# Kernel tuning notes

Measured on AMD Instinct MI355X. Metric: run time of the kernel, lower is better.

Reference implementation:

```python
import jax, jax.numpy as jnp
import numpy as np

N = 100000      # num POIs (nodes)
M = 20000       # num trajectories (hyperedges)
NNZ = 1000000   # incidence entries
D = 128         # emb_dim
NUM_LAYERS = 3
NEG_SLOPE = 0.2  # PyG HypergraphConv leaky_relu default


def setup_inputs() -> dict:
    key = jax.random.key(0)
    ks = jax.random.split(key, 8)
    pois_embs = jax.random.normal(ks[0], (N, D), jnp.float32)
    traj_embs = jax.random.normal(ks[1], (M, D), jnp.float32)
    hyperedge_weight = jax.random.uniform(ks[2], (M,), jnp.float32)
    node_idx = jax.random.randint(ks[3], (NNZ,), 0, N, jnp.int32)
    edge_idx = jax.random.randint(ks[4], (NNZ,), 0, M, jnp.int32)
    # learned params of the shared HypergraphConv layer (heads=1, concat)
    W_lin = jax.random.normal(ks[5], (D, D), jnp.float32) / np.sqrt(D).astype(np.float32)
    att = jax.random.normal(ks[6], (2 * D,), jnp.float32) * 0.1
    bias = jnp.zeros((D,), jnp.float32)
    return dict(pois_embs=pois_embs, traj_embs=traj_embs,
                hyperedge_weight=hyperedge_weight,
                node_idx=node_idx, edge_idx=edge_idx,
                W_lin=W_lin, att=att, bias=bias)


def _segment_softmax(scores, seg, num_seg):
    smax = jax.ops.segment_max(scores, seg, num_segments=num_seg)
    smax = jnp.where(jnp.isfinite(smax), smax, 0.0)  # guard empty segments
    ex = jnp.exp(scores - smax[seg])
    den = jax.ops.segment_sum(ex, seg, num_segments=num_seg)
    return ex / (den[seg] + 1e-16)


def _hconv(x, traj_embs, hyperedge_weight, node_idx, edge_idx, W_lin, att, bias):
    # x: [N, D] node feats; traj_embs: [M, D] hyperedge feats
    xt = x @ W_lin            # [N, D]  lin(x)
    et = traj_embs @ W_lin    # [M, D]  lin(hyperedge_attr)
    # attention logits per incidence pair (additive decomposition of cat*att)
    s_n = xt @ att[:D]        # [N]
    s_e = et @ att[D:]        # [M]
    alpha = jax.nn.leaky_relu(s_n[node_idx] + s_e[edge_idx], NEG_SLOPE)  # [NNZ]
    alpha = _segment_softmax(alpha, node_idx, N)  # softmax grouped by node
    # degree normalizations: D = sum_e H_ve * w_e, B = |e|
    Ddeg = jax.ops.segment_sum(hyperedge_weight[edge_idx], node_idx, num_segments=N)
    Dinv = jnp.where(Ddeg > 0, 1.0 / Ddeg, 0.0)
    Bdeg = jax.ops.segment_sum(jnp.ones((NNZ,), xt.dtype), edge_idx, num_segments=M)
    Binv = jnp.where(Bdeg > 0, 1.0 / Bdeg, 0.0)
    # node -> edge: B^{-1} H^T (alpha * x)
    msg1 = (alpha * Binv[edge_idx])[:, None] * xt[node_idx]        # [NNZ, D]
    edge_out = jax.ops.segment_sum(msg1, edge_idx, num_segments=M)  # [M, D]
    # edge -> node: D^{-1} H (alpha * edge_out)
    msg2 = (alpha * Dinv[node_idx])[:, None] * edge_out[edge_idx]   # [NNZ, D]
    out = jax.ops.segment_sum(msg2, node_idx, num_segments=N)       # [N, D]
    return out + bias


def reference(pois_embs, traj_embs, hyperedge_weight, node_idx, edge_idx, W_lin, att, bias):
    cur = pois_embs
    acc = pois_embs  # running sum of stacked layer outputs (incl. input)
    for _ in range(NUM_LAYERS):
        cur = _hconv(cur, traj_embs, hyperedge_weight, node_idx, edge_idx, W_lin, att, bias) + cur
        acc = acc + cur
    return acc / jnp.asarray(NUM_LAYERS + 1, acc.dtype)  # mean over stack
```

## Files before the change

kernel.cpp:

```cpp
#include <hip/hip_runtime.h>
#include <cstdint>
#include <cstddef>

#define DIM 128
#define NEG_SLOPE 0.2f

#define EREP 16
#define NREP 8

typedef __attribute__((ext_vector_type(8))) short short8v;
typedef __attribute__((ext_vector_type(4))) float float4v;

__device__ __forceinline__ float bf_lo(uint u) { return __uint_as_float(u << 16); }
__device__ __forceinline__ float bf_hi(uint u) { return __uint_as_float(u & 0xffff0000u); }
__device__ __forceinline__ uint f2bf(float f) {
  uint u = __float_as_uint(f);
  return (u + 0x7fffu + ((u >> 16) & 1u)) >> 16;
}
__device__ __forceinline__ uint pack_bf2(float lo, float hi) {
  return f2bf(lo) | (f2bf(hi) << 16);
}
__device__ __forceinline__ float lrelu(float x) {
  return x >= 0.0f ? x : NEG_SLOPE * x;
}

__global__ void wswz_kernel(const float* __restrict__ W, ushort* __restrict__ Wswz)
{
  int i = blockIdx.x * 256 + threadIdx.x;
  int j = i & 7, lane = (i >> 3) & 63, nt = (i >> 9) & 7, kt = i >> 12;
  int k = kt * 32 + (lane >> 4) * 8 + j;
  int col = nt * 16 + (lane & 15);
  Wswz[i] = (ushort)f2bf(W[k * 128 + col]);
}

__global__ void poisbf_kernel(const float* __restrict__ pois,
                              uint4* __restrict__ pois_bf, int N_, int NP)
{
  int i = blockIdx.x * 256 + threadIdx.x;
  if (i >= NP * 16) return;
  int row = i >> 4;
  uint4 o;
  if (row < N_) {
    const float* src = pois + (size_t)i * 8;
    float4 f0 = *(const float4*)src;
    float4 f1 = *(const float4*)(src + 4);
    o.x = pack_bf2(f0.x, f0.y); o.y = pack_bf2(f0.z, f0.w);
    o.z = pack_bf2(f1.x, f1.y); o.w = pack_bf2(f1.z, f1.w);
  } else { o.x = o.y = o.z = o.w = 0; }
  pois_bf[i] = o;
}

__global__ __launch_bounds__(256) void gemm_mfma_kernel(
    const ushort* __restrict__ Xb, const ushort* __restrict__ Wswz,
    const float* __restrict__ att, ushort* __restrict__ Yb,
    float* __restrict__ s_n, int rowsN)
{
  __shared__ ushort st[64 * 128];
  int tid = threadIdx.x;
  int w = tid >> 6, lane = tid & 63;
  int q = lane >> 4, c = lane & 15;
  int r0b = blockIdx.x * 64;
  int r0 = r0b + w * 16;
  float4v acc[8];
#pragma unroll
  for (int nt = 0; nt < 8; ++nt) acc[nt] = (float4v){0.f, 0.f, 0.f, 0.f};
  const ushort* arow = Xb + (size_t)(r0 + c) * DIM + q * 8;
#pragma unroll
  for (int kt = 0; kt < 4; ++kt) {
    short8v a = *(const short8v*)(arow + kt * 32);
#pragma unroll
    for (int nt = 0; nt < 8; ++nt) {
      short8v b = *(const short8v*)(Wswz + ((((kt << 3) + nt) << 9) + (lane << 3)));
      acc[nt] = __builtin_amdgcn_mfma_f32_16x16x32_bf16(a, b, acc[nt], 0, 0, 0);
    }
  }
  float av[8];
#pragma unroll
  for (int nt = 0; nt < 8; ++nt) av[nt] = att[nt * 16 + c];
  float p0 = 0, p1 = 0, p2 = 0, p3 = 0;
#pragma unroll
  for (int nt = 0; nt < 8; ++nt) {
    p0 = fmaf(acc[nt][0], av[nt], p0);
    p1 = fmaf(acc[nt][1], av[nt], p1);
    p2 = fmaf(acc[nt][2], av[nt], p2);
    p3 = fmaf(acc[nt][3], av[nt], p3);
  }
#pragma unroll
  for (int m = 8; m >= 1; m >>= 1) {
    p0 += __shfl_xor(p0, m, 64);
    p1 += __shfl_xor(p1, m, 64);
    p2 += __shfl_xor(p2, m, 64);
    p3 += __shfl_xor(p3, m, 64);
  }
  if (c == 0) {
    int rb = r0 + q * 4;
    if (rb + 0 < rowsN) s_n[rb + 0] = p0;
    if (rb + 1 < rowsN) s_n[rb + 1] = p1;
    if (rb + 2 < rowsN) s_n[rb + 2] = p2;
    if (rb + 3 < rowsN) s_n[rb + 3] = p3;
  }
  ushort* sw = st + w * 2048;
#pragma unroll
  for (int nt = 0; nt < 8; ++nt) {
    sw[(q * 4 + 0) * 128 + nt * 16 + c] = (ushort)f2bf(acc[nt][0]);
    sw[(q * 4 + 1) * 128 + nt * 16 + c] = (ushort)f2bf(acc[nt][1]);
    sw[(q * 4 + 2) * 128 + nt * 16 + c] = (ushort)f2bf(acc[nt][2]);
    sw[(q * 4 + 3) * 128 + nt * 16 + c] = (ushort)f2bf(acc[nt][3]);
  }
  __syncthreads();
#pragma unroll
  for (int it = 0; it < 4; ++it) {
    int idx = tid + it * 256;
    int row = idx >> 4, seg = idx & 15;
    *(uint4*)(Yb + (size_t)(r0b + row) * DIM + seg * 8) =
        *(const uint4*)&st[row * 128 + seg * 8];
  }
}

__global__ __launch_bounds__(256) void se_kernel(
    const float* __restrict__ traj, const float* __restrict__ W,
    const float* __restrict__ att, const float* __restrict__ hw,
    float* __restrict__ s_e, float2* __restrict__ se_hw, int M_)
{
  __shared__ float wv[128];
  int tid = threadIdx.x;
  if (tid < 128) {
    const float* wr = W + (size_t)tid * 128;
    float acc = 0.0f;
#pragma unroll 4
    for (int k = 0; k < 128; ++k) acc = fmaf(wr[k], att[DIM + k], acc);
    wv[tid] = acc;
  }
  __syncthreads();
  int e = blockIdx.x * 4 + (tid >> 6);
  int lane = tid & 63;
  if (e >= M_) return;
  const float* row = traj + (size_t)e * DIM;
  float v = row[lane] * wv[lane] + row[lane + 64] * wv[lane + 64];
#pragma unroll
  for (int d = 32; d > 0; d >>= 1) v += __shfl_down(v, d, 64);
  if (lane == 0) {
    s_e[e] = v;
    float2 g; g.x = v; g.y = hw[e];
    se_hw[e] = g;
  }
}

__global__ void hist_rank_kernel(const int* __restrict__ node_idx,
                                 const int* __restrict__ edge_idx,
                                 int* __restrict__ ncnt_r, int* __restrict__ ecnt_r,
                                 int* __restrict__ r_n, int* __restrict__ r_e,
                                 int nnz, int M_, int N_)
{
  int t = blockIdx.x * blockDim.x + threadIdx.x;
  int j = t * 2;
  if (j >= nnz) return;
  int* ec = ecnt_r + (size_t)(t & (EREP - 1)) * M_;
  int* nc = ncnt_r + (size_t)(t & (NREP - 1)) * N_;
  if (j + 2 <= nnz) {
    int2 e = *(const int2*)&edge_idx[j];
    int2 n = *(const int2*)&node_idx[j];
    int a0 = atomicAdd(&ec[e.x], 1);
    int a1 = atomicAdd(&ec[e.y], 1);
    int b0 = atomicAdd(&nc[n.x], 1);
    int b1 = atomicAdd(&nc[n.y], 1);
    *(int2*)&r_e[j] = make_int2(a0, a1);
    *(int2*)&r_n[j] = make_int2(b0, b1);
  } else {
    r_e[j] = atomicAdd(&ec[edge_idx[j]], 1);
    r_n[j] = atomicAdd(&nc[node_idx[j]], 1);
  }
}

__global__ void repsum_kernel(int* __restrict__ cnt_r, int* __restrict__ cnt,
                              int nbins, int reps)
{
  int b = blockIdx.x * blockDim.x + threadIdx.x;
  if (b >= nbins) return;
  int s = 0;
  for (int r = 0; r < reps; ++r) {
    size_t o = (size_t)r * nbins + b;
    int v = cnt_r[o];
    cnt_r[o] = s;
    s += v;
  }
  cnt[b] = s;
}

__global__ __launch_bounds__(1024) void scan_block_kernel(
    const int* __restrict__ cnt, int* __restrict__ off,
    int* __restrict__ partials, int nbins)
{
  __shared__ int ws[16];
  int tid = threadIdx.x, lane = tid & 63, wid = tid >> 6;
  int base = blockIdx.x * 4096 + tid * 4;
  int x0 = base + 0 < nbins ? cnt[base + 0] : 0;
  int x1 = base + 1 < nbins ? cnt[base + 1] : 0;
  int x2 = base + 2 < nbins ? cnt[base + 2] : 0;
  int x3 = base + 3 < nbins ? cnt[base + 3] : 0;
  int t = x0 + x1 + x2 + x3;
  int v = t;
#pragma unroll
  for (int d = 1; d < 64; d <<= 1) {
    int y = __shfl_up(v, d, 64);
    if (lane >= d) v += y;
  }
  if (lane == 63) ws[wid] = v;
  __syncthreads();
  if (tid < 16) {
    int s = ws[tid];
#pragma unroll
    for (int d = 1; d < 16; d <<= 1) {
      int y = __shfl_up(s, d, 16);
      if (tid >= d) s += y;
    }
    ws[tid] = s;
  }
  __syncthreads();
  int pre = (wid > 0 ? ws[wid - 1] : 0) + (v - t);
  if (base + 0 < nbins) off[base + 0] = pre;
  if (base + 1 < nbins) off[base + 1] = pre + x0;
  if (base + 2 < nbins) off[base + 2] = pre + x0 + x1;
  if (base + 3 < nbins) off[base + 3] = pre + x0 + x1 + x2;
  if (tid == 0) partials[blockIdx.x] = ws[15];
}

__global__ __launch_bounds__(64) void scan_partials_kernel(
    int* __restrict__ partials, int nb)
{
  int lane = threadIdx.x;
  int t = lane < nb ? partials[lane] : 0;
  int v = t;
#pragma unroll
  for (int d = 1; d < 64; d <<= 1) {
    int y = __shfl_up(v, d, 64);
    if (lane >= d) v += y;
  }
  if (lane < nb) partials[lane] = v - t;
  if (lane == 63) partials[nb] = v;
}

__global__ void add_off_combine_kernel(int* __restrict__ off,
                                       const int* __restrict__ partials,
                                       int* __restrict__ pre,
                                       int nbins, int nb, int reps)
{
  int i = blockIdx.x * blockDim.x + threadIdx.x;
  if (i < nbins) {
    int o = off[i] + partials[i >> 12];
    off[i] = o;
    for (int r = 0; r < reps; ++r) pre[(size_t)r * nbins + i] += o;
  }
  if (i == 0) off[nbins] = partials[nb];
}

__global__ void scatter_edge_kernel(const int* __restrict__ node_idx,
                                    const int* __restrict__ edge_idx,
                                    const int* __restrict__ r_e,
                                    const int* __restrict__ pre_e,
                                    int* __restrict__ nd_e, int nnz, int M_)
{
  int j = (blockIdx.x * blockDim.x + threadIdx.x) * 4;
  if (j >= nnz) return;
  if (j + 4 <= nnz) {
    const int* p0 = pre_e + (size_t)((j >> 1) & (EREP - 1)) * M_;
    const int* p1 = pre_e + (size_t)(((j >> 1) + 1) & (EREP - 1)) * M_;
    int4 e = *(const int4*)&edge_idx[j];
    int4 n = *(const int4*)&node_idx[j];
    int4 re = *(const int4*)&r_e[j];
    nd_e[p0[e.x] + re.x] = n.x;
    nd_e[p0[e.y] + re.y] = n.y;
    nd_e[p1[e.z] + re.z] = n.z;
    nd_e[p1[e.w] + re.w] = n.w;
  } else {
    for (int k = j; k < nnz; ++k) {
      const int* pp = pre_e + (size_t)((k >> 1) & (EREP - 1)) * M_;
      nd_e[pp[edge_idx[k]] + r_e[k]] = node_idx[k];
    }
  }
}

__global__ void scatter_node_kernel(const int* __restrict__ node_idx,
                                    const int* __restrict__ edge_idx,
                                    const int* __restrict__ r_n,
                                    const int* __restrict__ pre_n,
                                    int* __restrict__ eidx_n, int nnz, int N_)
{
  int j = (blockIdx.x * blockDim.x + threadIdx.x) * 4;
  if (j >= nnz) return;
  if (j + 4 <= nnz) {
    const int* p0 = pre_n + (size_t)((j >> 1) & (NREP - 1)) * N_;
    const int* p1 = pre_n + (size_t)(((j >> 1) + 1) & (NREP - 1)) * N_;
    int4 e = *(const int4*)&edge_idx[j];
    int4 n = *(const int4*)&node_idx[j];
    int4 rn = *(const int4*)&r_n[j];
    eidx_n[p0[n.x] + rn.x] = e.x;
    eidx_n[p0[n.y] + rn.y] = e.y;
    eidx_n[p1[n.z] + rn.z] = e.z;
    eidx_n[p1[n.w] + rn.w] = e.w;
  } else {
    for (int k = j; k < nnz; ++k) {
      const int* pp = pre_n + (size_t)((k >> 1) & (NREP - 1)) * N_;
      eidx_n[pp[node_idx[k]] + r_n[k]] = edge_idx[k];
    }
  }
}

__global__ void softstat_kernel(const int* __restrict__ noff,
                                const int* __restrict__ eidx_n,
                                const float* __restrict__ s_n,
                                const float2* __restrict__ se_hw,
                                float2* __restrict__ ns2,
                                float* __restrict__ Dinv, int N_)
{
  int n = blockIdx.x * blockDim.x + threadIdx.x;
  if (n >= N_) return;
  int s = noff[n], e1 = noff[n + 1];
  float sn = s_n[n];
  float m = -INFINITY, den = 0.0f, d = 0.0f;
  int t = s;
  for (; t + 4 <= e1; t += 4) {
    int i0 = eidx_n[t], i1 = eidx_n[t + 1], i2 = eidx_n[t + 2], i3 = eidx_n[t + 3];
    float2 g0 = se_hw[i0], g1 = se_hw[i1], g2 = se_hw[i2], g3 = se_hw[i3];
    float l0 = lrelu(sn + g0.x), l1 = lrelu(sn + g1.x);
    float l2 = lrelu(sn + g2.x), l3 = lrelu(sn + g3.x);
    float mm = fmaxf(fmaxf(fmaxf(l0, l1), fmaxf(l2, l3)), m);
    den = den * __expf(m - mm) + __expf(l0 - mm) + __expf(l1 - mm)
        + __expf(l2 - mm) + __expf(l3 - mm);
    m = mm;
    d += g0.y + g1.y + g2.y + g3.y;
  }
  for (; t < e1; ++t) {
    float2 g = se_hw[eidx_n[t]];
    float l = lrelu(sn + g.x);
    float mm = fmaxf(l, m);
    den = den * __expf(m - mm) + __expf(l - mm);
    m = mm;
    d += g.y;
  }
  if (s == e1) m = 0.0f;
  float2 r;
  r.x = sn;
  r.y = m + __logf(den + 1e-16f);
  ns2[n] = r;
  Dinv[n] = d > 0.0f ? 1.0f / d : 0.0f;
}

__global__ __launch_bounds__(256) void msg1_kernel(
    const int* __restrict__ eoff, const int* __restrict__ nd_e,
    const float2* __restrict__ ns2, const float* __restrict__ s_e,
    const ushort* __restrict__ xt, uint* __restrict__ eo, int M_)
{
  int e = blockIdx.x * (blockDim.x >> 6) + (threadIdx.x >> 6);
  int lane = threadIdx.x & 63;
  if (e >= M_) return;
  int s = eoff[e], t1 = eoff[e + 1];
  int len = t1 - s;
  float binv = len > 0 ? 1.0f / (float)len : 0.0f;
  float se = s_e[e];
  const uint* xt4 = (const uint*)xt + lane;
  float2 acc = {0.0f, 0.0f};
  int t = s;
  for (; t + 8 <= t1; t += 8) {
    int n0 = nd_e[t],     n1 = nd_e[t + 1], n2 = nd_e[t + 2], n3 = nd_e[t + 3];
    int n4 = nd_e[t + 4], n5 = nd_e[t + 5], n6 = nd_e[t + 6], n7 = nd_e[t + 7];
    float2 q0 = ns2[n0], q1 = ns2[n1], q2 = ns2[n2], q3 = ns2[n3];
    float2 q4 = ns2[n4], q5 = ns2[n5], q6 = ns2[n6], q7 = ns2[n7];
    uint u0 = xt4[(size_t)n0 * 64], u1 = xt4[(size_t)n1 * 64];
    uint u2 = xt4[(size_t)n2 * 64], u3 = xt4[(size_t)n3 * 64];
    uint u4 = xt4[(size_t)n4 * 64], u5 = xt4[(size_t)n5 * 64];
    uint u6 = xt4[(size_t)n6 * 64], u7 = xt4[(size_t)n7 * 64];
    float c0 = __expf(lrelu(q0.x + se) - q0.y);
    float c1 = __expf(lrelu(q1.x + se) - q1.y);
    float c2 = __expf(lrelu(q2.x + se) - q2.y);
    float c3 = __expf(lrelu(q3.x + se) - q3.y);
    float c4 = __expf(lrelu(q4.x + se) - q4.y);
    float c5 = __expf(lrelu(q5.x + se) - q5.y);
    float c6 = __expf(lrelu(q6.x + se) - q6.y);
    float c7 = __expf(lrelu(q7.x + se) - q7.y);
    acc.x = fmaf(c0, bf_lo(u0), acc.x); acc.y = fmaf(c0, bf_hi(u0), acc.y);
    acc.x = fmaf(c1, bf_lo(u1), acc.x); acc.y = fmaf(c1, bf_hi(u1), acc.y);
    acc.x = fmaf(c2, bf_lo(u2), acc.x); acc.y = fmaf(c2, bf_hi(u2), acc.y);
    acc.x = fmaf(c3, bf_lo(u3), acc.x); acc.y = fmaf(c3, bf_hi(u3), acc.y);
    acc.x = fmaf(c4, bf_lo(u4), acc.x); acc.y = fmaf(c4, bf_hi(u4), acc.y);
    acc.x = fmaf(c5, bf_lo(u5), acc.x); acc.y = fmaf(c5, bf_hi(u5), acc.y);
    acc.x = fmaf(c6, bf_lo(u6), acc.x); acc.y = fmaf(c6, bf_hi(u6), acc.y);
    acc.x = fmaf(c7, bf_lo(u7), acc.x); acc.y = fmaf(c7, bf_hi(u7), acc.y);
  }
  for (; t < t1; ++t) {
    int nd = nd_e[t];
    float2 q = ns2[nd];
    uint u = xt4[(size_t)nd * 64];
    float c = __expf(lrelu(q.x + se) - q.y);
    acc.x = fmaf(c, bf_lo(u), acc.x);
    acc.y = fmaf(c, bf_hi(u), acc.y);
  }
  eo[(size_t)e * (DIM / 2) + lane] = pack_bf2(acc.x * binv, acc.y * binv);
}

__global__ __launch_bounds__(256) void msg2_kernel(
    const int* __restrict__ noff, const int* __restrict__ eidx_n,
    const float2* __restrict__ ns2, const float* __restrict__ Dinv,
    const float* __restrict__ s_e, const uint* __restrict__ eo,
    const float* __restrict__ bias,
    const float* __restrict__ cur_in, const float* __restrict__ acc_in,
    float* __restrict__ cur_out, uint* __restrict__ curbf_out,
    float* __restrict__ acc_out, int last, int N_)
{
  int n = blockIdx.x * (blockDim.x >> 6) + (threadIdx.x >> 6);
  int lane = threadIdx.x & 63;
  if (n >= N_) return;
  int s = noff[n], t1 = noff[n + 1];
  float2 nsv = ns2[n];
  float sn = nsv.x, lz = nsv.y;
  const uint* eo4 = eo + lane;
  float2 acc = {0.0f, 0.0f};
  int t = s;
  for (; t + 8 <= t1; t += 8) {
    int e0 = eidx_n[t],     e1 = eidx_n[t + 1], e2 = eidx_n[t + 2], e3 = eidx_n[t + 3];
    int e4 = eidx_n[t + 4], e5 = eidx_n[t + 5], e6 = eidx_n[t + 6], e7 = eidx_n[t + 7];
    float x0 = s_e[e0], x1 = s_e[e1], x2 = s_e[e2], x3 = s_e[e3];
    float x4 = s_e[e4], x5 = s_e[e5], x6 = s_e[e6], x7 = s_e[e7];
    uint u0 = eo4[(size_t)e0 * 64], u1 = eo4[(size_t)e1 * 64];
    uint u2 = eo4[(size_t)e2 * 64], u3 = eo4[(size_t)e3 * 64];
    uint u4 = eo4[(size_t)e4 * 64], u5 = eo4[(size_t)e5 * 64];
    uint u6 = eo4[(size_t)e6 * 64], u7 = eo4[(size_t)e7 * 64];
    float c0 = __expf(lrelu(sn + x0) - lz);
    float c1 = __expf(lrelu(sn + x1) - lz);
    float c2 = __expf(lrelu(sn + x2) - lz);
    float c3 = __expf(lrelu(sn + x3) - lz);
    float c4 = __expf(lrelu(sn + x4) - lz);
    float c5 = __expf(lrelu(sn + x5) - lz);
    float c6 = __expf(lrelu(sn + x6) - lz);
    float c7 = __expf(lrelu(sn + x7) - lz);
    acc.x = fmaf(c0, bf_lo(u0), acc.x); acc.y = fmaf(c0, bf_hi(u0), acc.y);
    acc.x = fmaf(c1, bf_lo(u1), acc.x); acc.y = fmaf(c1, bf_hi(u1), acc.y);
    acc.x = fmaf(c2, bf_lo(u2), acc.x); acc.y = fmaf(c2, bf_hi(u2), acc.y);
    acc.x = fmaf(c3, bf_lo(u3), acc.x); acc.y = fmaf(c3, bf_hi(u3), acc.y);
    acc.x = fmaf(c4, bf_lo(u4), acc.x); acc.y = fmaf(c4, bf_hi(u4), acc.y);
    acc.x = fmaf(c5, bf_lo(u5), acc.x); acc.y = fmaf(c5, bf_hi(u5), acc.y);
    acc.x = fmaf(c6, bf_lo(u6), acc.x); acc.y = fmaf(c6, bf_hi(u6), acc.y);
    acc.x = fmaf(c7, bf_lo(u7), acc.x); acc.y = fmaf(c7, bf_hi(u7), acc.y);
  }
  for (; t < t1; ++t) {
    int e = eidx_n[t];
    uint u = eo4[(size_t)e * 64];
    float c = __expf(lrelu(sn + s_e[e]) - lz);
    acc.x = fmaf(c, bf_lo(u), acc.x);
    acc.y = fmaf(c, bf_hi(u), acc.y);
  }
  float sc = Dinv[n];
  float2 b = ((const float2*)bias)[lane];
  size_t idx = (size_t)n * DIM + lane * 2;
  float cx = cur_in[idx]     + acc.x * sc + b.x;
  float cy = cur_in[idx + 1] + acc.y * sc + b.y;
  if (last) {
    acc_out[idx]     = (acc_in[idx]     + cx) * 0.25f;
    acc_out[idx + 1] = (acc_in[idx + 1] + cy) * 0.25f;
  } else {
    cur_out[idx] = cx; cur_out[idx + 1] = cy;
    curbf_out[(size_t)n * 64 + lane] = pack_bf2(cx, cy);
    acc_out[idx]     = acc_in[idx]     + cx;
    acc_out[idx + 1] = acc_in[idx + 1] + cy;
  }
}

static inline int cdiv(int a, int b) { return (a + b - 1) / b; }

extern "C" void kernel_launch(void* const* d_in, const int* in_sizes, int n_in,
                              void* d_out, int out_size, void* d_ws, size_t ws_size,
                              hipStream_t stream)
{
  const float* pois = (const float*)d_in[0];
  const float* traj = (const float*)d_in[1];
  const float* hw   = (const float*)d_in[2];
  const int* node_idx = (const int*)d_in[3];
  const int* edge_idx = (const int*)d_in[4];
  const float* W    = (const float*)d_in[5];
  const float* att  = (const float*)d_in[6];
  const float* bias = (const float*)d_in[7];
  float* dout = (float*)d_out;

  const int N   = in_sizes[0] / DIM;
  const int M   = in_sizes[2];
  const int NNZ = in_sizes[3];
  const int NP  = (N + 63) & ~63;

  char* p = (char*)d_ws;
  auto alloc = [&](size_t bytes) -> void* {
    void* r = (void*)p;
    p += (bytes + 255) & ~(size_t)255;
    return r;
  };
  ushort* xt_bf   = (ushort*)alloc((size_t)NP * DIM * 2);
  ushort* cur_bf  = (ushort*)alloc((size_t)NP * DIM * 2);
  ushort* pois_bf = (ushort*)alloc((size_t)NP * DIM * 2);
  ushort* W_swz   = (ushort*)alloc(16384 * 2);
  uint*   eo_bf = (uint*)alloc((size_t)M * (DIM / 2) * 4);
  float*  cur   = (float*)alloc((size_t)N * DIM * 4);
  float2* ns2   = (float2*)alloc((size_t)N * 8);
  float*  s_e  = (float*)alloc((size_t)M * 4);
  float2* se_hw = (float2*)alloc((size_t)M * 8);
  float*  s_n  = (float*)alloc((size_t)N * 4);
  float*  Dinv = (float*)alloc((size_t)N * 4);
  int* ecnt   = (int*)alloc((size_t)M * 4);
  int* ncnt   = (int*)alloc((size_t)N * 4);
  int* ecnt_r = (int*)alloc((size_t)EREP * M * 4);
  int* ncnt_r = (int*)alloc((size_t)NREP * N * 4);
  int* eoff = (int*)alloc((size_t)(M + 1) * 4);
  int* noff = (int*)alloc((size_t)(N + 1) * 4);
  int* r_e  = (int*)alloc((size_t)NNZ * 4);
  int* r_n  = (int*)alloc((size_t)NNZ * 4);
  int* nd_e   = (int*)alloc((size_t)NNZ * 4);
  int* eidx_n = (int*)alloc((size_t)NNZ * 4);
  int* part_e = (int*)alloc(65 * 4);
  int* part_n = (int*)alloc(65 * 4);
  (void)ws_size;

  const int nbE = cdiv(M, 4096), nbN = cdiv(N, 4096);

  hipMemsetAsync(ecnt_r, 0, (size_t)EREP * M * 4, stream);
  hipMemsetAsync(ncnt_r, 0, (size_t)NREP * N * 4, stream);
  hist_rank_kernel<<<cdiv(NNZ, 512), 256, 0, stream>>>(node_idx, edge_idx, ncnt_r, ecnt_r, r_n, r_e, NNZ, M, N);
  repsum_kernel<<<cdiv(M, 256), 256, 0, stream>>>(ecnt_r, ecnt, M, EREP);
  repsum_kernel<<<cdiv(N, 256), 256, 0, stream>>>(ncnt_r, ncnt, N, NREP);
  scan_block_kernel<<<nbE, 1024, 0, stream>>>(ecnt, eoff, part_e, M);
  scan_block_kernel<<<nbN, 1024, 0, stream>>>(ncnt, noff, part_n, N);
  scan_partials_kernel<<<1, 64, 0, stream>>>(part_e, nbE);
  scan_partials_kernel<<<1, 64, 0, stream>>>(part_n, nbN);
  add_off_combine_kernel<<<cdiv(M, 256), 256, 0, stream>>>(eoff, part_e, ecnt_r, M, nbE, EREP);
  add_off_combine_kernel<<<cdiv(N, 256), 256, 0, stream>>>(noff, part_n, ncnt_r, N, nbN, NREP);
  scatter_edge_kernel<<<cdiv(NNZ, 1024), 256, 0, stream>>>(node_idx, edge_idx, r_e, ecnt_r, nd_e, NNZ, M);
  scatter_node_kernel<<<cdiv(NNZ, 1024), 256, 0, stream>>>(node_idx, edge_idx, r_n, ncnt_r, eidx_n, NNZ, N);

  wswz_kernel<<<64, 256, 0, stream>>>(W, W_swz);
  se_kernel<<<cdiv(M, 4), 256, 0, stream>>>(traj, W, att, hw, s_e, se_hw, M);
  poisbf_kernel<<<cdiv(NP * 16, 256), 256, 0, stream>>>(pois, (uint4*)pois_bf, N, NP);

  for (int layer = 0; layer < 3; ++layer) {
    const ushort* gin = (layer == 0) ? pois_bf : cur_bf;
    gemm_mfma_kernel<<<NP / 64, 256, 0, stream>>>(gin, W_swz, att, xt_bf, s_n, N);
    softstat_kernel<<<cdiv(N, 256), 256, 0, stream>>>(noff, eidx_n, s_n, se_hw, ns2, Dinv, N);
    msg1_kernel<<<cdiv(M, 4), 256, 0, stream>>>(eoff, nd_e, ns2, s_e, xt_bf, eo_bf, M);
    const float* cin = (layer == 0) ? pois : cur;
    const float* ain = (layer == 0) ? pois : dout;
    int last = (layer == 2) ? 1 : 0;
    msg2_kernel<<<cdiv(N, 4), 256, 0, stream>>>(noff, eidx_n, ns2, Dinv, s_e, eo_bf,
                                                bias, cin, ain, cur, (uint*)cur_bf,
                                                dout, last, N);
  }
}
```

Baseline: 754.9 us.

## Precompute softmax alphas per node and broadcast coefficients via readlane in gathers

softstat now writes the per-incidence softmax coefficients into an NNZ-sized alpha_n array in node-sorted order. msg2 reads these coefficients directly instead of gathering s_e and recomputing exp per lane. Both msg1 and msg2 now load indices and coefficients cooperatively, one per lane, and broadcast them with readlane. This removes redundant per-lane scalar gathers and exp work. It adds extra global writes and reads of alpha_n in softstat, and the readlane loop may limit memory-level parallelism compared with the explicit 8-way unroll.

```diff
diff --git a/kernel.cpp b/kernel.cpp
--- a/kernel.cpp
+++ b/kernel.cpp
@@ -311,7 +311,8 @@
                                 const float* __restrict__ s_n,
                                 const float2* __restrict__ se_hw,
                                 float2* __restrict__ ns2,
-                                float* __restrict__ Dinv, int N_)
+                                float* __restrict__ Dinv,
+                                float* __restrict__ alpha_n, int N_)
 {
   int n = blockIdx.x * blockDim.x + threadIdx.x;
   if (n >= N_) return;
@@ -324,6 +325,7 @@
     float2 g0 = se_hw[i0], g1 = se_hw[i1], g2 = se_hw[i2], g3 = se_hw[i3];
     float l0 = lrelu(sn + g0.x), l1 = lrelu(sn + g1.x);
     float l2 = lrelu(sn + g2.x), l3 = lrelu(sn + g3.x);
+    alpha_n[t] = l0; alpha_n[t + 1] = l1; alpha_n[t + 2] = l2; alpha_n[t + 3] = l3;
     float mm = fmaxf(fmaxf(fmaxf(l0, l1), fmaxf(l2, l3)), m);
     den = den * __expf(m - mm) + __expf(l0 - mm) + __expf(l1 - mm)
         + __expf(l2 - mm) + __expf(l3 - mm);
@@ -333,17 +335,27 @@
   for (; t < e1; ++t) {
     float2 g = se_hw[eidx_n[t]];
     float l = lrelu(sn + g.x);
+    alpha_n[t] = l;
     float mm = fmaxf(l, m);
     den = den * __expf(m - mm) + __expf(l - mm);
     m = mm;
     d += g.y;
   }
   if (s == e1) m = 0.0f;
+  float lz = m + __logf(den + 1e-16f);
   float2 r;
   r.x = sn;
-  r.y = m + __logf(den + 1e-16f);
+  r.y = lz;
   ns2[n] = r;
   Dinv[n] = d > 0.0f ? 1.0f / d : 0.0f;
+  for (t = s; t + 4 <= e1; t += 4) {
+    float l0 = alpha_n[t], l1 = alpha_n[t + 1], l2 = alpha_n[t + 2], l3 = alpha_n[t + 3];
+    alpha_n[t]     = __expf(l0 - lz);
+    alpha_n[t + 1] = __expf(l1 - lz);
+    alpha_n[t + 2] = __expf(l2 - lz);
+    alpha_n[t + 3] = __expf(l3 - lz);
+  }
+  for (; t < e1; ++t) alpha_n[t] = __expf(alpha_n[t] - lz);
 }
 
 __global__ __launch_bounds__(256) void msg1_kernel(
@@ -360,49 +372,31 @@
   float se = s_e[e];
   const uint* xt4 = (const uint*)xt + lane;
   float2 acc = {0.0f, 0.0f};
-  int t = s;
-  for (; t + 8 <= t1; t += 8) {
-    int n0 = nd_e[t],     n1 = nd_e[t + 1], n2 = nd_e[t + 2], n3 = nd_e[t + 3];
-    int n4 = nd_e[t + 4], n5 = nd_e[t + 5], n6 = nd_e[t + 6], n7 = nd_e[t + 7];
-    float2 q0 = ns2[n0], q1 = ns2[n1], q2 = ns2[n2], q3 = ns2[n3];
-    float2 q4 = ns2[n4], q5 = ns2[n5], q6 = ns2[n6], q7 = ns2[n7];
-    uint u0 = xt4[(size_t)n0 * 64], u1 = xt4[(size_t)n1 * 64];
-    uint u2 = xt4[(size_t)n2 * 64], u3 = xt4[(size_t)n3 * 64];
-    uint u4 = xt4[(size_t)n4 * 64], u5 = xt4[(size_t)n5 * 64];
-    uint u6 = xt4[(size_t)n6 * 64], u7 = xt4[(size_t)n7 * 64];
-    float c0 = __expf(lrelu(q0.x + se) - q0.y);
-    float c1 = __expf(lrelu(q1.x + se) - q1.y);
-    float c2 = __expf(lrelu(q2.x + se) - q2.y);
-    float c3 = __expf(lrelu(q3.x + se) - q3.y);
-    float c4 = __expf(lrelu(q4.x + se) - q4.y);
-    float c5 = __expf(lrelu(q5.x + se) - q5.y);
-    float c6 = __expf(lrelu(q6.x + se) - q6.y);
-    float c7 = __expf(lrelu(q7.x + se) - q7.y);
-    acc.x = fmaf(c0, bf_lo(u0), acc.x); acc.y = fmaf(c0, bf_hi(u0), acc.y);
-    acc.x = fmaf(c1, bf_lo(u1), acc.x); acc.y = fmaf(c1, bf_hi(u1), acc.y);
-    acc.x = fmaf(c2, bf_lo(u2), acc.x); acc.y = fmaf(c2, bf_hi(u2), acc.y);
-    acc.x = fmaf(c3, bf_lo(u3), acc.x); acc.y = fmaf(c3, bf_hi(u3), acc.y);
-    acc.x = fmaf(c4, bf_lo(u4), acc.x); acc.y = fmaf(c4, bf_hi(u4), acc.y);
-    acc.x = fmaf(c5, bf_lo(u5), acc.x); acc.y = fmaf(c5, bf_hi(u5), acc.y);
-    acc.x = fmaf(c6, bf_lo(u6), acc.x); acc.y = fmaf(c6, bf_hi(u6), acc.y);
-    acc.x = fmaf(c7, bf_lo(u7), acc.x); acc.y = fmaf(c7, bf_hi(u7), acc.y);
-  }
-  for (; t < t1; ++t) {
-    int nd = nd_e[t];
-    float2 q = ns2[nd];
-    uint u = xt4[(size_t)nd * 64];
-    float c = __expf(lrelu(q.x + se) - q.y);
-    acc.x = fmaf(c, bf_lo(u), acc.x);
-    acc.y = fmaf(c, bf_hi(u), acc.y);
+  for (int base = s; base < t1; base += 64) {
+    int rem = t1 - base;
+    int cnt = rem < 64 ? rem : 64;
+    int nd = 0; float cl = 0.0f;
+    if (lane < cnt) {
+      nd = nd_e[base + lane];
+      float2 q = ns2[nd];
+      cl = __expf(lrelu(q.x + se) - q.y);
+    }
+#pragma unroll 4
+    for (int i = 0; i < cnt; ++i) {
+      int ndi = __builtin_amdgcn_readlane(nd, i);
+      float ci = __uint_as_float(__builtin_amdgcn_readlane(__float_as_uint(cl), i));
+      uint u = xt4[(size_t)ndi * 64];
+      acc.x = fmaf(ci, bf_lo(u), acc.x);
+      acc.y = fmaf(ci, bf_hi(u), acc.y);
+    }
   }
   eo[(size_t)e * (DIM / 2) + lane] = pack_bf2(acc.x * binv, acc.y * binv);
 }
 
 __global__ __launch_bounds__(256) void msg2_kernel(
     const int* __restrict__ noff, const int* __restrict__ eidx_n,
-    const float2* __restrict__ ns2, const float* __restrict__ Dinv,
-    const float* __restrict__ s_e, const uint* __restrict__ eo,
-    const float* __restrict__ bias,
+    const float* __restrict__ alpha_n, const float* __restrict__ Dinv,
+    const uint* __restrict__ eo, const float* __restrict__ bias,
     const float* __restrict__ cur_in, const float* __restrict__ acc_in,
     float* __restrict__ cur_out, uint* __restrict__ curbf_out,
     float* __restrict__ acc_out, int last, int N_)
@@ -411,43 +405,24 @@
   int lane = threadIdx.x & 63;
   if (n >= N_) return;
   int s = noff[n], t1 = noff[n + 1];
-  float2 nsv = ns2[n];
-  float sn = nsv.x, lz = nsv.y;
   const uint* eo4 = eo + lane;
   float2 acc = {0.0f, 0.0f};
-  int t = s;
-  for (; t + 8 <= t1; t += 8) {
-    int e0 = eidx_n[t],     e1 = eidx_n[t + 1], e2 = eidx_n[t + 2], e3 = eidx_n[t + 3];
-    int e4 = eidx_n[t + 4], e5 = eidx_n[t + 5], e6 = eidx_n[t + 6], e7 = eidx_n[t + 7];
-    float x0 = s_e[e0], x1 = s_e[e1], x2 = s_e[e2], x3 = s_e[e3];
-    float x4 = s_e[e4], x5 = s_e[e5], x6 = s_e[e6], x7 = s_e[e7];
-    uint u0 = eo4[(size_t)e0 * 64], u1 = eo4[(size_t)e1 * 64];
-    uint u2 = eo4[(size_t)e2 * 64], u3 = eo4[(size_t)e3 * 64];
-    uint u4 = eo4[(size_t)e4 * 64], u5 = eo4[(size_t)e5 * 64];
-    uint u6 = eo4[(size_t)e6 * 64], u7 = eo4[(size_t)e7 * 64];
-    float c0 = __expf(lrelu(sn + x0) - lz);
-    float c1 = __expf(lrelu(sn + x1) - lz);
-    float c2 = __expf(lrelu(sn + x2) - lz);
-    float c3 = __expf(lrelu(sn + x3) - lz);
-    float c4 = __expf(lrelu(sn + x4) - lz);
-    float c5 = __expf(lrelu(sn + x5) - lz);
-    float c6 = __expf(lrelu(sn + x6) - lz);
-    float c7 = __expf(lrelu(sn + x7) - lz);
-    acc.x = fmaf(c0, bf_lo(u0), acc.x); acc.y = fmaf(c0, bf_hi(u0), acc.y);
-    acc.x = fmaf(c1, bf_lo(u1), acc.x); acc.y = fmaf(c1, bf_hi(u1), acc.y);
-    acc.x = fmaf(c2, bf_lo(u2), acc.x); acc.y = fmaf(c2, bf_hi(u2), acc.y);
-    acc.x = fmaf(c3, bf_lo(u3), acc.x); acc.y = fmaf(c3, bf_hi(u3), acc.y);
-    acc.x = fmaf(c4, bf_lo(u4), acc.x); acc.y = fmaf(c4, bf_hi(u4), acc.y);
-    acc.x = fmaf(c5, bf_lo(u5), acc.x); acc.y = fmaf(c5, bf_hi(u5), acc.y);
-    acc.x = fmaf(c6, bf_lo(u6), acc.x); acc.y = fmaf(c6, bf_hi(u6), acc.y);
-    acc.x = fmaf(c7, bf_lo(u7), acc.x); acc.y = fmaf(c7, bf_hi(u7), acc.y);
-  }
-  for (; t < t1; ++t) {
-    int e = eidx_n[t];
-    uint u = eo4[(size_t)e * 64];
-    float c = __expf(lrelu(sn + s_e[e]) - lz);
-    acc.x = fmaf(c, bf_lo(u), acc.x);
-    acc.y = fmaf(c, bf_hi(u), acc.y);
+  for (int base = s; base < t1; base += 64) {
+    int rem = t1 - base;
+    int cnt = rem < 64 ? rem : 64;
+    int el = 0; float cl = 0.0f;
+    if (lane < cnt) {
+      el = eidx_n[base + lane];
+      cl = alpha_n[base + lane];
+    }
+#pragma unroll 4
+    for (int i = 0; i < cnt; ++i) {
+      int ei = __builtin_amdgcn_readlane(el, i);
+      float ci = __uint_as_float(__builtin_amdgcn_readlane(__float_as_uint(cl), i));
+      uint u = eo4[(size_t)ei * 64];
+      acc.x = fmaf(ci, bf_lo(u), acc.x);
+      acc.y = fmaf(ci, bf_hi(u), acc.y);
+    }
   }
   float sc = Dinv[n];
   float2 b = ((const float2*)bias)[lane];
@@ -503,6 +478,7 @@
   float2* se_hw = (float2*)alloc((size_t)M * 8);
   float*  s_n  = (float*)alloc((size_t)N * 4);
   float*  Dinv = (float*)alloc((size_t)N * 4);
+  float*  alpha_n = (float*)alloc((size_t)NNZ * 4);
   int* ecnt   = (int*)alloc((size_t)M * 4);
   int* ncnt   = (int*)alloc((size_t)N * 4);
   int* ecnt_r = (int*)alloc((size_t)EREP * M * 4);
@@ -540,12 +516,12 @@
   for (int layer = 0; layer < 3; ++layer) {
     const ushort* gin = (layer == 0) ? pois_bf : cur_bf;
     gemm_mfma_kernel<<<NP / 64, 256, 0, stream>>>(gin, W_swz, att, xt_bf, s_n, N);
-    softstat_kernel<<<cdiv(N, 256), 256, 0, stream>>>(noff, eidx_n, s_n, se_hw, ns2, Dinv, N);
+    softstat_kernel<<<cdiv(N, 256), 256, 0, stream>>>(noff, eidx_n, s_n, se_hw, ns2, Dinv, alpha_n, N);
     msg1_kernel<<<cdiv(M, 4), 256, 0, stream>>>(eoff, nd_e, ns2, s_e, xt_bf, eo_bf, M);
     const float* cin = (layer == 0) ? pois : cur;
     const float* ain = (layer == 0) ? pois : dout;
     int last = (layer == 2) ? 1 : 0;
-    msg2_kernel<<<cdiv(N, 4), 256, 0, stream>>>(noff, eidx_n, ns2, Dinv, s_e, eo_bf,
+    msg2_kernel<<<cdiv(N, 4), 256, 0, stream>>>(noff, eidx_n, alpha_n, Dinv, eo_bf,
                                                 bias, cin, ain, cur, (uint*)cur_bf,
                                                 dout, last, N);
   }
```

New measurement: 833.1 us. +10.4%, slower.
